# Performance work log

Measured on AMD Instinct MI355X. Metric: run time of the kernel, lower is better.

## Reference

```python
import jax, jax.numpy as jnp
import numpy as np

SEQ_LEN = 8192
HEAD_DIM = 128


def setup_inputs() -> dict:
    key = jax.random.key(0)
    kq, kk, kv = jax.random.split(key, 3)
    q = jax.random.normal(kq, (SEQ_LEN, HEAD_DIM), dtype=jnp.float32)
    k = jax.random.normal(kk, (SEQ_LEN, HEAD_DIM), dtype=jnp.float32)
    v = jax.random.normal(kv, (SEQ_LEN, HEAD_DIM), dtype=jnp.float32)
    return {"q": q, "k": k, "v": v}


def reference(q, k, v):
    # FlashAttention computes exact softmax attention; the blocked loops with
    # online max/sum rescaling in the source are an exact reformulation of:
    #   O = softmax(Q K^T) V
    # NOTE: the original module applies no 1/sqrt(d) scaling, so neither do we.
    s = jnp.einsum('nd,md->nm', q, k)          # [N, N] scores
    p = jax.nn.softmax(s, axis=-1)             # stable softmax (online in src)
    return jnp.einsum('nm,md->nd', p, v)       # [N, d]
```

## Files before the change

### kernel.cpp

```cpp
#include <hip/hip_runtime.h>

#define N_SEQ 8192
#define HDIM  128

typedef _Float16 half8v  __attribute__((ext_vector_type(8)));
typedef float    floatx16 __attribute__((ext_vector_type(16)));
typedef unsigned int uint32;

__global__ void prep_kv(const float* __restrict__ K, const float* __restrict__ V,
                        _Float16* __restrict__ K16s, _Float16* __restrict__ Vs) {
    __shared__ float Kl[32 * 132];
    __shared__ float Vl[32 * 132];
    const int t  = threadIdx.x;
    const int nt = blockIdx.x;
    const int n0 = nt * 32;
    #pragma unroll
    for (int kk = 0; kk < 4; kk++) {
        int idx = t + 256 * kk;
        int nl = idx >> 5, c4 = idx & 31;
        float4 f = *(((const float4*)(K + (size_t)(n0 + nl) * HDIM)) + c4);
        float* dk = &Kl[nl * 132 + c4 * 4];
        dk[0] = f.x; dk[1] = f.y; dk[2] = f.z; dk[3] = f.w;
        float4 g = *(((const float4*)(V + (size_t)(n0 + nl) * HDIM)) + c4);
        float* dv = &Vl[nl * 132 + c4 * 4];
        dv[0] = g.x; dv[1] = g.y; dv[2] = g.z; dv[3] = g.w;
    }
    __syncthreads();
    #pragma unroll
    for (int rep = 0; rep < 2; rep++) {
        int ch = t + rep * 256;
        int kc = ch >> 6, lane = ch & 63, l31 = lane & 31, q5 = (lane >> 5) & 1;
        half8v h;
        #pragma unroll
        for (int j = 0; j < 8; j++) h[j] = (_Float16)Kl[l31 * 132 + kc * 16 + q5 * 8 + j];
        *(half8v*)(K16s + (((size_t)nt * 8 + kc) * 64 + lane) * 8) = h;
    }
    #pragma unroll
    for (int rep = 0; rep < 2; rep++) {
        int ch = t + rep * 256;
        int dt = ch >> 7, kc2 = (ch >> 6) & 1, lane = ch & 63, l31 = lane & 31, q5 = (lane >> 5) & 1;
        half8v h;
        #pragma unroll
        for (int j = 0; j < 8; j++) h[j] = (_Float16)Vl[(kc2 * 16 + q5 * 8 + j) * 132 + dt * 32 + l31];
        *(half8v*)(Vs + ((((size_t)nt * 4 + dt) * 2 + kc2) * 64 + lane) * 8) = h;
    }
}

static __device__ __forceinline__ void stage_tile(
        const _Float16* __restrict__ K16s, const _Float16* __restrict__ Vs,
        _Float16* lds, size_t nt, int wv, int lane) {
    #pragma unroll
    for (int i = 0; i < 4; i++) {
        const int c = wv * 4 + i;
        const _Float16* base = (c < 8) ? (K16s + (nt * 8 + c) * 512)
                                       : (Vs + (nt * 8 + (size_t)(c - 8)) * 512);
        __builtin_amdgcn_global_load_lds(
            (const __attribute__((address_space(1))) void*)(base + lane * 8),
            (__attribute__((address_space(3))) void*)(lds + c * 512),
            16, 0, 0);
    }
}

static __device__ __forceinline__ void do_pv(const half8v (&vsrc)[8], const uint32 (&hpk)[8],
                                             floatx16 (&oacc)[4], int q5) {
    #pragma unroll
    for (int kc2 = 0; kc2 < 2; kc2++) {
        uint32 pass0 = q5 ? hpk[4 * kc2 + 0] : hpk[4 * kc2 + 2];
        uint32 pass1 = q5 ? hpk[4 * kc2 + 1] : hpk[4 * kc2 + 3];
        uint32 r0 = (uint32)__shfl_xor((int)pass0, 32, 64);
        uint32 r1 = (uint32)__shfl_xor((int)pass1, 32, 64);
        uint32 b0 = q5 ? r0 : hpk[4 * kc2 + 0];
        uint32 b1 = q5 ? r1 : hpk[4 * kc2 + 1];
        uint32 b2 = q5 ? hpk[4 * kc2 + 2] : r0;
        uint32 b3 = q5 ? hpk[4 * kc2 + 3] : r1;
        uint4 bu = make_uint4(b0, b1, b2, b3);
        half8v bfrag = __builtin_bit_cast(half8v, bu);
        #pragma unroll
        for (int dt = 0; dt < 4; dt++)
            oacc[dt] = __builtin_amdgcn_mfma_f32_32x32x16_f16(vsrc[dt * 2 + kc2], bfrag, oacc[dt], 0, 0, 0);
    }
}

static __device__ __forceinline__ void step64(
        const half8v (&qf)[8], floatx16 (&oacc)[4],
        float& runm, float& lsum,
        const _Float16* lds, int lane, int q5) {
    half8v kf[8];
    #pragma unroll
    for (int kc = 0; kc < 8; kc++)
        kf[kc] = *(const half8v*)(lds + kc * 512 + lane * 8);
    floatx16 s0, s1;
    #pragma unroll
    for (int r = 0; r < 16; r++) { s0[r] = 0.0f; s1[r] = 0.0f; }
    #pragma unroll
    for (int kc = 0; kc < 4; kc++)
        s0 = __builtin_amdgcn_mfma_f32_32x32x16_f16(kf[kc], qf[kc], s0, 0, 0, 0);
    #pragma unroll
    for (int kc = 4; kc < 8; kc++)
        s1 = __builtin_amdgcn_mfma_f32_32x32x16_f16(kf[kc], qf[kc], s1, 0, 0, 0);
    float sA[16];
    #pragma unroll
    for (int r = 0; r < 16; r++) sA[r] = s0[r] + s1[r];
    #pragma unroll
    for (int kc = 0; kc < 8; kc++)
        kf[kc] = *(const half8v*)(lds + 8192 + kc * 512 + lane * 8);
    #pragma unroll
    for (int r = 0; r < 16; r++) { s0[r] = 0.0f; s1[r] = 0.0f; }
    #pragma unroll
    for (int kc = 0; kc < 4; kc++)
        s0 = __builtin_amdgcn_mfma_f32_32x32x16_f16(kf[kc], qf[kc], s0, 0, 0, 0);
    #pragma unroll
    for (int kc = 4; kc < 8; kc++)
        s1 = __builtin_amdgcn_mfma_f32_32x32x16_f16(kf[kc], qf[kc], s1, 0, 0, 0);
    float sB[16];
    #pragma unroll
    for (int r = 0; r < 16; r++) sB[r] = s0[r] + s1[r];
    float tm[8];
    #pragma unroll
    for (int r = 0; r < 8; r++)
        tm[r] = fmaxf(fmaxf(sA[r], sA[r + 8]), fmaxf(sB[r], sB[r + 8]));
    #pragma unroll
    for (int w = 4; w; w >>= 1)
        #pragma unroll
        for (int r = 0; r < w; r++) tm[r] = fmaxf(tm[r], tm[r + w]);
    float cmax = fmaxf(tm[0], __shfl_xor(tm[0], 32, 64));
    if (__any(cmax > runm + 12.0f)) {
        const float mnew = fmaxf(runm, cmax);
        const float alpha = __builtin_amdgcn_exp2f(runm - mnew);
        #pragma unroll
        for (int dt = 0; dt < 4; dt++)
            #pragma unroll
            for (int r = 0; r < 16; r++) oacc[dt][r] *= alpha;
        lsum *= alpha;
        runm = mnew;
    }
    float pA[16], pB[16];
    #pragma unroll
    for (int r = 0; r < 16; r++) pA[r] = __builtin_amdgcn_exp2f(sA[r] - runm);
    #pragma unroll
    for (int r = 0; r < 16; r++) pB[r] = __builtin_amdgcn_exp2f(sB[r] - runm);
    float ts[8];
    #pragma unroll
    for (int r = 0; r < 8; r++) ts[r] = (pA[r] + pA[r + 8]) + (pB[r] + pB[r + 8]);
    #pragma unroll
    for (int w = 4; w; w >>= 1)
        #pragma unroll
        for (int r = 0; r < w; r++) ts[r] += ts[r + w];
    lsum += ts[0];
    uint32 hA[8], hB[8];
    #pragma unroll
    for (int t2 = 0; t2 < 8; t2++) {
        auto ka = __builtin_amdgcn_cvt_pkrtz(pA[2 * t2], pA[2 * t2 + 1]);
        hA[t2] = __builtin_bit_cast(uint32, ka);
        auto kb = __builtin_amdgcn_cvt_pkrtz(pB[2 * t2], pB[2 * t2 + 1]);
        hB[t2] = __builtin_bit_cast(uint32, kb);
    }
    #pragma unroll
    for (int j = 0; j < 8; j++)
        kf[j] = *(const half8v*)(lds + (8 + j) * 512 + lane * 8);
    do_pv(kf, hA, oacc, q5);
    #pragma unroll
    for (int j = 0; j < 8; j++)
        kf[j] = *(const half8v*)(lds + 8192 + (8 + j) * 512 + lane * 8);
    do_pv(kf, hB, oacc, q5);
}

__launch_bounds__(256, 2)
__global__ void fa_main(const float* __restrict__ Qp, const _Float16* __restrict__ K16s,
                        const _Float16* __restrict__ Vs, _Float16* __restrict__ Opart,
                        float* __restrict__ lpart, float* __restrict__ mpart, int tiles) {
    __shared__ _Float16 ldsbuf[2][16384];
    const int tid  = threadIdx.x;
    const int lane = tid & 63;
    const int wv   = tid >> 6;
    const int l31  = lane & 31;
    const int q5   = lane >> 5;
    const int sp   = blockIdx.x;
    const int m0   = blockIdx.y * 128 + wv * 32;
    const float LOG2E = 1.44269504088896f;

    half8v qf[8];
    {
        const float* qrow = Qp + (size_t)(m0 + l31) * HDIM;
        #pragma unroll
        for (int kc = 0; kc < 8; kc++) {
            const float4 a = *(const float4*)(qrow + kc * 16 + q5 * 8);
            const float4 b = *(const float4*)(qrow + kc * 16 + q5 * 8 + 4);
            half8v h;
            h[0] = (_Float16)(a.x * LOG2E); h[1] = (_Float16)(a.y * LOG2E);
            h[2] = (_Float16)(a.z * LOG2E); h[3] = (_Float16)(a.w * LOG2E);
            h[4] = (_Float16)(b.x * LOG2E); h[5] = (_Float16)(b.y * LOG2E);
            h[6] = (_Float16)(b.z * LOG2E); h[7] = (_Float16)(b.w * LOG2E);
            qf[kc] = h;
        }
    }

    floatx16 oacc[4];
    #pragma unroll
    for (int dt = 0; dt < 4; dt++)
        #pragma unroll
        for (int r = 0; r < 16; r++) oacc[dt][r] = 0.0f;

    float runm = -3.0e38f;
    float lsum = 0.0f;

    const size_t nt0 = (size_t)sp * tiles;
    const int phases = tiles >> 1;

    stage_tile(K16s, Vs, ldsbuf[0], nt0 + 0, wv, lane);
    stage_tile(K16s, Vs, ldsbuf[0] + 8192, nt0 + 1, wv, lane);
    __syncthreads();
    for (int ph = 0; ph < phases; ph++) {
        _Float16* cur = ldsbuf[ph & 1];
        _Float16* nxt = ldsbuf[(ph & 1) ^ 1];
        if (ph + 1 < phases) {
            stage_tile(K16s, Vs, nxt, nt0 + 2 * ph + 2, wv, lane);
            stage_tile(K16s, Vs, nxt + 8192, nt0 + 2 * ph + 3, wv, lane);
        }
        step64(qf, oacc, runm, lsum, cur, lane, q5);
        __syncthreads();
    }

    float ltot = lsum + __shfl_xor(lsum, 32, 64);
    if (lane < 32) {
        lpart[(size_t)sp * N_SEQ + m0 + l31] = ltot;
        mpart[(size_t)sp * N_SEQ + m0 + l31] = runm;
    }

    float* ldsf = (float*)ldsbuf;
    const size_t obase = ((size_t)sp * N_SEQ + blockIdx.y * 128) * HDIM;
    #pragma unroll
    for (int qtr = 0; qtr < 4; qtr++) {
        __syncthreads();
        if (wv == qtr) {
            #pragma unroll
            for (int dt = 0; dt < 4; dt++)
                #pragma unroll
                for (int g = 0; g < 4; g++) {
                    float4 v = make_float4(oacc[dt][4 * g + 0], oacc[dt][4 * g + 1],
                                           oacc[dt][4 * g + 2], oacc[dt][4 * g + 3]);
                    *(float4*)&ldsf[l31 * 132 + dt * 32 + g * 8 + q5 * 4] = v;
                }
        }
        __syncthreads();
        const int lrow = wv * 8 + (lane >> 3);
        const int c    = lane & 7;
        const float* row = &ldsf[lrow * 132 + c * 16];
        uint32 w0[4];
        #pragma unroll
        for (int j = 0; j < 4; j++) {
            auto pk = __builtin_amdgcn_cvt_pkrtz(row[2 * j], row[2 * j + 1]);
            w0[j] = __builtin_bit_cast(uint32, pk);
        }
        uint32 w1[4];
        #pragma unroll
        for (int j = 0; j < 4; j++) {
            auto pk = __builtin_amdgcn_cvt_pkrtz(row[8 + 2 * j], row[8 + 2 * j + 1]);
            w1[j] = __builtin_bit_cast(uint32, pk);
        }
        _Float16* dst = Opart + obase + (size_t)(qtr * 32 + lrow) * HDIM + c * 16;
        *(half8v*)(dst)     = __builtin_bit_cast(half8v, make_uint4(w0[0], w0[1], w0[2], w0[3]));
        *(half8v*)(dst + 8) = __builtin_bit_cast(half8v, make_uint4(w1[0], w1[1], w1[2], w1[3]));
    }
}

template <int S>
__global__ __launch_bounds__(256) void fa_merge(const _Float16* __restrict__ Opart,
                                                const float* __restrict__ lpart,
                                                const float* __restrict__ mpart,
                                                float* __restrict__ Out) {
    const int t = threadIdx.x;
    const int m = blockIdx.x * 32 + (t >> 3);
    const int c = t & 7;

    float mv[S], lv[S];
    #pragma unroll
    for (int s = 0; s < S; s++) {
        mv[s] = mpart[(size_t)s * N_SEQ + m];
        lv[s] = lpart[(size_t)s * N_SEQ + m];
    }
    float M = -3.0e38f;
    #pragma unroll
    for (int s = 0; s < S; s++) M = fmaxf(M, mv[s]);
    float wsc[S];
    float L = 0.0f;
    #pragma unroll
    for (int s = 0; s < S; s++) {
        wsc[s] = __builtin_amdgcn_exp2f(mv[s] - M);
        L += lv[s] * wsc[s];
    }
    const float inv = 1.0f / L;

    float acc[16];
    #pragma unroll
    for (int j = 0; j < 16; j++) acc[j] = 0.0f;
    #pragma unroll
    for (int s = 0; s < S; s++) {
        const float ww = wsc[s] * inv;
        const _Float16* src = Opart + ((size_t)s * N_SEQ + m) * HDIM + c * 16;
        half8v h0 = *(const half8v*)(src);
        half8v h1 = *(const half8v*)(src + 8);
        #pragma unroll
        for (int j = 0; j < 8; j++) acc[j]     += (float)h0[j] * ww;
        #pragma unroll
        for (int j = 0; j < 8; j++) acc[8 + j] += (float)h1[j] * ww;
    }
    float* dst = Out + (size_t)m * HDIM + c * 16;
    #pragma unroll
    for (int j = 0; j < 4; j++) {
        float4 v = make_float4(acc[4 * j], acc[4 * j + 1], acc[4 * j + 2], acc[4 * j + 3]);
        *(float4*)(dst + 4 * j) = v;
    }
}

__global__ void fa_naive(const float* __restrict__ Q, const float* __restrict__ K,
                         const float* __restrict__ V, float* __restrict__ O) {
    const int m = blockIdx.x;
    const int t = threadIdx.x;
    __shared__ float qs[HDIM];
    __shared__ float ps[256];
    __shared__ float red[256];
    if (t < HDIM) qs[t] = Q[(size_t)m * HDIM + t] * 1.44269504f;
    __syncthreads();
    float om = -3.0e38f, ls = 0.0f, oa = 0.0f;
    for (int nb = 0; nb < N_SEQ; nb += 256) {
        const float* kr = K + (size_t)(nb + t) * HDIM;
        float s = 0.0f;
        #pragma unroll 8
        for (int d = 0; d < HDIM; d++) s += qs[d] * kr[d];
        red[t] = s; __syncthreads();
        for (int st = 128; st > 0; st >>= 1) { if (t < st) red[t] = fmaxf(red[t], red[t + st]); __syncthreads(); }
        float cm = red[0];
        __syncthreads();
        float mn = fmaxf(om, cm);
        float al = __builtin_amdgcn_exp2f(om - mn);
        om = mn;
        float pp = __builtin_amdgcn_exp2f(s - mn);
        ps[t] = pp; red[t] = pp; __syncthreads();
        for (int st = 128; st > 0; st >>= 1) { if (t < st) red[t] += red[t + st]; __syncthreads(); }
        float csum = red[0];
        ls = ls * al + csum;
        if (t < HDIM) {
            float acc = 0.0f;
            for (int j = 0; j < 256; j++) acc += ps[j] * V[(size_t)(nb + j) * HDIM + t];
            oa = oa * al + acc;
        }
        __syncthreads();
    }
    if (t < HDIM) O[(size_t)m * HDIM + t] = oa / ls;
}

extern "C" void kernel_launch(void* const* d_in, const int* in_sizes, int n_in,
                              void* d_out, int out_size, void* d_ws, size_t ws_size,
                              hipStream_t stream) {
    const float* q = (const float*)d_in[0];
    const float* k = (const float*)d_in[1];
    const float* v = (const float*)d_in[2];
    float* out = (float*)d_out;

    const size_t MB = 1024ull * 1024ull;
    int S = 0;
    for (int s = 8; s >= 1; s >>= 1) {
        size_t need = 4 * MB + (size_t)s * (2 * MB + 64 * 1024);
        if (ws_size >= need) { S = s; break; }
    }
    if (S == 0) {
        fa_naive<<<N_SEQ, 256, 0, stream>>>(q, k, v, out);
        return;
    }
    char* ws = (char*)d_ws;
    _Float16* K16s = (_Float16*)ws;
    _Float16* Vs   = (_Float16*)(ws + 2 * MB);
    _Float16* Opart = (_Float16*)(ws + 4 * MB);
    float* lpart   = (float*)(ws + 4 * MB + (size_t)S * 2 * MB);
    float* mpart   = lpart + (size_t)S * N_SEQ;

    prep_kv<<<dim3(N_SEQ / 32), dim3(256), 0, stream>>>(k, v, K16s, Vs);
    fa_main<<<dim3(S, N_SEQ / 128), dim3(256), 0, stream>>>(q, K16s, Vs, Opart, lpart, mpart, (N_SEQ / 32) / S);
    dim3 mg(N_SEQ / 32);
    switch (S) {
        case 8:  fa_merge<8> <<<mg, dim3(256), 0, stream>>>(Opart, lpart, mpart, out); break;
        case 4:  fa_merge<4> <<<mg, dim3(256), 0, stream>>>(Opart, lpart, mpart, out); break;
        case 2:  fa_merge<2> <<<mg, dim3(256), 0, stream>>>(Opart, lpart, mpart, out); break;
        default: fa_merge<1> <<<mg, dim3(256), 0, stream>>>(Opart, lpart, mpart, out); break;
    }
}
```

Baseline: 118.6 us.

## Fuse split-KV merge into main kernel via last-block atomic counter

Removes the separate fa_merge launch. Each fa_main block bumps a per-row-tile atomic counter after writing its partial results, and the last split block to finish merges all S partials into the output. Counters are zeroed in prep_kv. This saves a kernel launch and its tail, at the cost of threadfences, an atomic per block, and a serialized merge done by one block per row tile, with 2 threads per row instead of 8.

```diff
diff --git a/kernel.cpp b/kernel.cpp
--- a/kernel.cpp
+++ b/kernel.cpp
@@ -8,12 +8,14 @@
 typedef unsigned int uint32;
 
 __global__ void prep_kv(const float* __restrict__ K, const float* __restrict__ V,
-                        _Float16* __restrict__ K16s, _Float16* __restrict__ Vs) {
+                        _Float16* __restrict__ K16s, _Float16* __restrict__ Vs,
+                        int* __restrict__ counters) {
     __shared__ float Kl[32 * 132];
     __shared__ float Vl[32 * 132];
     const int t  = threadIdx.x;
     const int nt = blockIdx.x;
     const int n0 = nt * 32;
+    if (nt == 0 && t < 64) counters[t] = 0;
     #pragma unroll
     for (int kk = 0; kk < 4; kk++) {
         int idx = t + 256 * kk;
@@ -168,8 +170,10 @@
 __launch_bounds__(256, 2)
 __global__ void fa_main(const float* __restrict__ Qp, const _Float16* __restrict__ K16s,
                         const _Float16* __restrict__ Vs, _Float16* __restrict__ Opart,
-                        float* __restrict__ lpart, float* __restrict__ mpart, int tiles) {
+                        float* __restrict__ lpart, float* __restrict__ mpart,
+                        int* __restrict__ counters, float* __restrict__ Out, int tiles) {
     __shared__ _Float16 ldsbuf[2][16384];
+    __shared__ int flag_s;
     const int tid  = threadIdx.x;
     const int lane = tid & 63;
     const int wv   = tid >> 6;
@@ -262,54 +266,62 @@
         *(half8v*)(dst)     = __builtin_bit_cast(half8v, make_uint4(w0[0], w0[1], w0[2], w0[3]));
         *(half8v*)(dst + 8) = __builtin_bit_cast(half8v, make_uint4(w1[0], w1[1], w1[2], w1[3]));
     }
-}
-
-template <int S>
-__global__ __launch_bounds__(256) void fa_merge(const _Float16* __restrict__ Opart,
-                                                const float* __restrict__ lpart,
-                                                const float* __restrict__ mpart,
-                                                float* __restrict__ Out) {
-    const int t = threadIdx.x;
-    const int m = blockIdx.x * 32 + (t >> 3);
-    const int c = t & 7;
-
-    float mv[S], lv[S];
-    #pragma unroll
-    for (int s = 0; s < S; s++) {
-        mv[s] = mpart[(size_t)s * N_SEQ + m];
-        lv[s] = lpart[(size_t)s * N_SEQ + m];
-    }
+
+    __syncthreads();
+    if (tid == 0) {
+        __threadfence();
+        int old = atomicAdd(&counters[blockIdx.y], 1);
+        flag_s = (old == (int)gridDim.x - 1);
+    }
+    __syncthreads();
+    if (!flag_s) return;
+    __threadfence();
+
+    const int S   = gridDim.x;
+    const int ym0 = blockIdx.y * 128;
+    const int m   = ym0 + (tid >> 1);
+    float mv[8], lv[8];
+    #pragma unroll
+    for (int s = 0; s < 8; s++)
+        if (s < S) { mv[s] = mpart[(size_t)s * N_SEQ + m]; lv[s] = lpart[(size_t)s * N_SEQ + m]; }
     float M = -3.0e38f;
     #pragma unroll
-    for (int s = 0; s < S; s++) M = fmaxf(M, mv[s]);
-    float wsc[S];
+    for (int s = 0; s < 8; s++) if (s < S) M = fmaxf(M, mv[s]);
+    float wsc[8];
     float L = 0.0f;
     #pragma unroll
-    for (int s = 0; s < S; s++) {
-        wsc[s] = __builtin_amdgcn_exp2f(mv[s] - M);
-        L += lv[s] * wsc[s];
-    }
+    for (int s = 0; s < 8; s++)
+        if (s < S) { wsc[s] = __builtin_amdgcn_exp2f(mv[s] - M); L += lv[s] * wsc[s]; }
     const float inv = 1.0f / L;
-
-    float acc[16];
-    #pragma unroll
-    for (int j = 0; j < 16; j++) acc[j] = 0.0f;
-    #pragma unroll
-    for (int s = 0; s < S; s++) {
-        const float ww = wsc[s] * inv;
-        const _Float16* src = Opart + ((size_t)s * N_SEQ + m) * HDIM + c * 16;
-        half8v h0 = *(const half8v*)(src);
-        half8v h1 = *(const half8v*)(src + 8);
-        #pragma unroll
-        for (int j = 0; j < 8; j++) acc[j]     += (float)h0[j] * ww;
-        #pragma unroll
-        for (int j = 0; j < 8; j++) acc[8 + j] += (float)h1[j] * ww;
-    }
-    float* dst = Out + (size_t)m * HDIM + c * 16;
-    #pragma unroll
-    for (int j = 0; j < 4; j++) {
-        float4 v = make_float4(acc[4 * j], acc[4 * j + 1], acc[4 * j + 2], acc[4 * j + 3]);
-        *(float4*)(dst + 4 * j) = v;
+    #pragma unroll
+    for (int u = 0; u < 2; u++) {
+        const int d0 = (tid & 1) * 64 + u * 32;
+        float acc[32];
+        #pragma unroll
+        for (int j = 0; j < 32; j++) acc[j] = 0.0f;
+        #pragma unroll
+        for (int s = 0; s < 8; s++)
+            if (s < S) {
+                const float ww = wsc[s] * inv;
+                const _Float16* src = Opart + ((size_t)s * N_SEQ + m) * HDIM + d0;
+                half8v h0 = *(const half8v*)(src);
+                half8v h1 = *(const half8v*)(src + 8);
+                half8v h2 = *(const half8v*)(src + 16);
+                half8v h3 = *(const half8v*)(src + 24);
+                #pragma unroll
+                for (int j = 0; j < 8; j++) {
+                    acc[j]      += (float)h0[j] * ww;
+                    acc[8 + j]  += (float)h1[j] * ww;
+                    acc[16 + j] += (float)h2[j] * ww;
+                    acc[24 + j] += (float)h3[j] * ww;
+                }
+            }
+        float* dst = Out + (size_t)m * HDIM + d0;
+        #pragma unroll
+        for (int j = 0; j < 8; j++) {
+            float4 v = make_float4(acc[4 * j], acc[4 * j + 1], acc[4 * j + 2], acc[4 * j + 3]);
+            *(float4*)(dst + 4 * j) = v;
+        }
     }
 }
 
@@ -361,7 +373,7 @@
     const size_t MB = 1024ull * 1024ull;
     int S = 0;
     for (int s = 8; s >= 1; s >>= 1) {
-        size_t need = 4 * MB + (size_t)s * (2 * MB + 64 * 1024);
+        size_t need = 4 * MB + (size_t)s * (2 * MB + 64 * 1024) + 4096;
         if (ws_size >= need) { S = s; break; }
     }
     if (S == 0) {
@@ -374,14 +386,9 @@
     _Float16* Opart = (_Float16*)(ws + 4 * MB);
     float* lpart   = (float*)(ws + 4 * MB + (size_t)S * 2 * MB);
     float* mpart   = lpart + (size_t)S * N_SEQ;
-
-    prep_kv<<<dim3(N_SEQ / 32), dim3(256), 0, stream>>>(k, v, K16s, Vs);
-    fa_main<<<dim3(S, N_SEQ / 128), dim3(256), 0, stream>>>(q, K16s, Vs, Opart, lpart, mpart, (N_SEQ / 32) / S);
-    dim3 mg(N_SEQ / 32);
-    switch (S) {
-        case 8:  fa_merge<8> <<<mg, dim3(256), 0, stream>>>(Opart, lpart, mpart, out); break;
-        case 4:  fa_merge<4> <<<mg, dim3(256), 0, stream>>>(Opart, lpart, mpart, out); break;
-        case 2:  fa_merge<2> <<<mg, dim3(256), 0, stream>>>(Opart, lpart, mpart, out); break;
-        default: fa_merge<1> <<<mg, dim3(256), 0, stream>>>(Opart, lpart, mpart, out); break;
-    }
-}
+    int*   counters = (int*)(mpart + (size_t)S * N_SEQ);
+
+    prep_kv<<<dim3(N_SEQ / 32), dim3(256), 0, stream>>>(k, v, K16s, Vs, counters);
+    fa_main<<<dim3(S, N_SEQ / 128), dim3(256), 0, stream>>>(
+        q, K16s, Vs, Opart, lpart, mpart, counters, out, (N_SEQ / 32) / S);
+}
```

Result: slower. 168.9 us (+42.4%).
